# Optimization experiments

Hardware: AMD Instinct MI355X
Metric: run time of the kernel (lower is better)

The kernel has to match this reference:

```python
import jax, jax.numpy as jnp
import numpy as np

H = 16  # n_heads
D = 64  # d_keys


def setup_inputs() -> dict:
    key = jax.random.key(0)
    ks = jax.random.split(key, 11)
    b, n, dm = 2, 2048, 1024
    s = 1.0 / np.sqrt(dm)
    return {
        "q": jax.random.normal(ks[0], (b, n, dm), jnp.float32),
        "k": jax.random.normal(ks[1], (b, n, dm), jnp.float32),
        "v": jax.random.normal(ks[2], (b, n, dm), jnp.float32),
        "Wq": jax.random.normal(ks[3], (dm, H * D), jnp.float32) * s,
        "bq": jax.random.normal(ks[4], (H * D,), jnp.float32) * 0.01,
        "Wk": jax.random.normal(ks[5], (dm, H * D), jnp.float32) * s,
        "bk": jax.random.normal(ks[6], (H * D,), jnp.float32) * 0.01,
        "Wv": jax.random.normal(ks[7], (dm, H * D), jnp.float32) * s,
        "bv": jax.random.normal(ks[8], (H * D,), jnp.float32) * 0.01,
        "Wo": jax.random.normal(ks[9], (H * D, dm), jnp.float32) * s,
        "bo": jax.random.normal(ks[10], (dm,), jnp.float32) * 0.01,
    }


def reference(q, k, v, Wq, bq, Wk, bk, Wv, bv, Wo, bo):
    b, n_q, _ = q.shape
    n_k = k.shape[1]
    # projections -> [b, n, h, d]
    qh = (q @ Wq + bq).reshape(b, n_q, H, D)
    kh = (k @ Wk + bk).reshape(b, n_k, H, D)
    vh = (v @ Wv + bv).reshape(b, n_k, H, D)
    # scores [b, h, n, m]
    scores = jnp.einsum('bnhd,bmhd->bhnm', qh, kh)
    causal = jnp.triu(jnp.ones((n_q, n_k), dtype=bool), k=1)  # True above diag
    scores = jnp.where(causal, -jnp.inf, scores)
    att = jax.nn.softmax(scores / np.sqrt(D).astype(np.float32), axis=-1)
    att_out = jnp.einsum('bhnm,bmhd->bnhd', att, vh).reshape(b, n_q, H * D)
    return att_out @ Wo + bo
```

## Files before the change

### kernel.cpp

```cpp
#include <hip/hip_runtime.h>

typedef float f32x4 __attribute__((ext_vector_type(4)));
typedef __bf16 bf16x8 __attribute__((ext_vector_type(8)));
typedef __bf16 bf16x4 __attribute__((ext_vector_type(4)));
typedef __bf16 bf16_t;

#define NH 16
#define DH 64
#define SEQ 2048
#define DM 1024

#define QSCALE 0.18033688f

extern "C" hipError_t hipMemPtrGetInfo(void* ptr, size_t* size);

__device__ __forceinline__ bf16x8 ld8(const bf16_t* p) { return *(const bf16x8*)p; }
__device__ __forceinline__ void st8(bf16_t* p, bf16x8 v) { *(bf16x8*)p = v; }

__device__ __forceinline__ void gl_lds16(const bf16_t* g, bf16_t* l)
{
    __builtin_amdgcn_global_load_lds(
        (const __attribute__((address_space(1))) unsigned int*)g,
        (__attribute__((address_space(3))) unsigned int*)l, 16, 0, 0);
}

__global__ __launch_bounds__(256) void fill_sentinel(float* out, unsigned n, float val)
{
    unsigned stride = gridDim.x * blockDim.x;
    for (unsigned i = blockIdx.x * blockDim.x + threadIdx.x; i < n; i += stride)
        out[i] = val;
}

__global__ __launch_bounds__(256) void prep(
    const float* __restrict__ q, const float* __restrict__ k,
    const float* __restrict__ v,
    const float* __restrict__ w0, const float* __restrict__ w1,
    const float* __restrict__ w2, const float* __restrict__ w3,
    bf16_t* __restrict__ xb, bf16_t* __restrict__ wt, int fragmode)
{
    int z = blockIdx.z;
    if (z < 3) {
        const float* src = (z == 0) ? q : (z == 1) ? k : v;
        bf16_t* dst = xb + (size_t)z * (4096u * 1024u);
        size_t i8 = ((size_t)blockIdx.x * 256 + threadIdx.x) * 8;
        f32x4 u = *(const f32x4*)(src + i8);
        f32x4 w = *(const f32x4*)(src + i8 + 4);
        bf16x8 h = { (bf16_t)u.x, (bf16_t)u.y, (bf16_t)u.z, (bf16_t)u.w,
                     (bf16_t)w.x, (bf16_t)w.y, (bf16_t)w.z, (bf16_t)w.w };
        st8(dst + i8, h);
    } else {
        int x = blockIdx.x;
        if (x >= 1024) return;
        int w = x >> 8, rem = x & 255;
        int bx = rem & 15, by = rem >> 4;
        const float* in = (w == 0) ? w0 : (w == 1) ? w1 : (w == 2) ? w2 : w3;
        bf16_t* out = wt + (size_t)w * DM * DM;
        __shared__ __align__(16) bf16_t tile[64][72];
        int t = threadIdx.x;
        int k0 = by * 64, n0 = bx * 64;
        int r0 = t >> 4, c0 = (t & 15) * 4;
        for (int p = 0; p < 4; p++) {
            int r = r0 + p * 16;
            const float* src = in + (size_t)(k0 + r) * DM + n0 + c0;
            for (int i = 0; i < 4; i++) tile[r][c0 + i] = (bf16_t)src[i];
        }
        __syncthreads();
        if (fragmode) {
            int idx = t;
            #pragma unroll
            for (int p = 0; p < 2; p++, idx += 256) {
                int rn = idx & 63;
                int kc8 = idx >> 6;
                int n_abs = n0 + rn;
                int rblk = n_abs >> 4, l16v = n_abs & 15;
                int kk = kc8 >> 2, gg = kc8 & 3;
                bf16x8 vv;
                for (int j = 0; j < 8; j++) vv[j] = tile[kc8 * 8 + j][rn];
                st8(out + (size_t)((rblk * 16 + by) * 2 + kk) * 512
                        + (gg * 16 + l16v) * 8, vv);
            }
        } else {
            for (int p = 0; p < 4; p++) {
                int rn = r0 + p * 16;
                bf16_t* dst = out + (size_t)(n0 + rn) * DM + k0 + c0;
                for (int i = 0; i < 4; i++) dst[i] = tile[c0 + i][rn];
            }
        }
    }
}

#define LGKM0 asm volatile("s_waitcnt lgkmcnt(0)" ::: "memory")
#define VMC(n) asm volatile("s_waitcnt vmcnt(" #n ")" ::: "memory")
#define BARRIER __builtin_amdgcn_s_barrier()

#define STA(d, h, dk) do { \
    _Pragma("unroll") for (int j = 0; j < 2; j++) \
        gl_lds16(Xp + ((h) * 128 + j * 64) * DM + (dk) * 64, \
                 Ab + sdst0 + ((d) * 2 + (h)) * 8192 + j * 4096); } while (0)
#define RDA(d, h, F) do { \
    _Pragma("unroll") for (int mf = 0; mf < 4; mf++) { \
        F[mf][0] = ld8(Ab + rA0 + ((d) * 2 + (h)) * 8192 + mf * 1024); \
        F[mf][1] = ld8(Ab + rA1 + ((d) * 2 + (h)) * 8192 + mf * 1024); } } while (0)
#define LDB(SET, nh, kto) do { \
    _Pragma("unroll") for (int nf = 0; nf < 2; nf++) \
        _Pragma("unroll") for (int kk = 0; kk < 2; kk++) \
            SET[nf][kk] = ld8(Bp + (nh) * 131072 + nf * 16384 \
                              + (kto) * 1024 + kk * 512); } while (0)
#define MMQ(AF, BF, Q) do { \
    __builtin_amdgcn_s_setprio(1); \
    _Pragma("unroll") for (int mf = 0; mf < 4; mf++) \
        _Pragma("unroll") for (int nf = 0; nf < 2; nf++) { \
            Q[mf][nf] = __builtin_amdgcn_mfma_f32_16x16x32_bf16( \
                AF[mf][0], BF[nf][0], Q[mf][nf], 0, 0, 0); \
            Q[mf][nf] = __builtin_amdgcn_mfma_f32_16x16x32_bf16( \
                AF[mf][1], BF[nf][1], Q[mf][nf], 0, 0, 0); } \
    __builtin_amdgcn_s_setprio(0); } while (0)

__global__ __launch_bounds__(512, 2) void gemm8(
    const bf16_t* __restrict__ xall, const bf16_t* __restrict__ bfall,
    const float* __restrict__ b0v, const float* __restrict__ b1v,
    const float* __restrict__ b2v, bf16_t* __restrict__ outall,
    float* __restrict__ outf, int mode_base, int out_is_f32)
{
    int z = blockIdx.z;
    int mode = mode_base + z;
    int qkv = (mode_base == 0);
    const bf16_t* X  = xall  + (qkv ? (size_t)z * (4096u * 1024u) : 0);
    const bf16_t* Bf = bfall + (qkv ? (size_t)z * (1024u * 1024u) : 0);
    const float* bias = (z == 0) ? b0v : (z == 1) ? b1v : b2v;
    bf16_t* out = outall + (qkv ? (size_t)z * (4096u * 1024u) : 0);

    int m0 = blockIdx.x * 256;
    int n0 = blockIdx.y * 256;

    __shared__ __align__(16) bf16_t Ab[2 * 2 * 128 * 64];

    int tid  = threadIdx.x;
    int lane = tid & 63, w = tid >> 6;
    int g = lane >> 4, l16 = lane & 15;
    int wm = w >> 2, wn = w & 3;
    int rl = lane >> 3, cl = lane & 7;
    int w8 = w * 8;

    int srow = w8 + rl;
    int scol = (cl ^ rl) * 8;
    const bf16_t* Xp = X + (size_t)(m0 + srow) * DM + scol;
    int sdst0 = w8 * 64 + lane * 8;

    int x7 = l16 & 7;
    int rA0 = (wm * 64 + l16) * 64 + ((0 + g) ^ x7) * 8;
    int rA1 = (wm * 64 + l16) * 64 + ((4 + g) ^ x7) * 8;

    const bf16_t* Bp = Bf + ((size_t)(n0 >> 4) + wn * 2) * 16384 + lane * 8;

    f32x4 a00[4][2] = {}, a01[4][2] = {}, a10[4][2] = {}, a11[4][2] = {};
    bf16x8 afA[4][2], afB[4][2], Ba[2][2], Bb[2][2];

    STA(0, 0, 0); STA(0, 1, 0); STA(1, 0, 1); STA(1, 1, 1);
    LDB(Ba, 0, 0); LDB(Bb, 1, 0);
    VMC(0);
    BARRIER;
    RDA(0, 0, afA);

    #pragma unroll 1
    for (int i = 0; i < 7; i++) {
        VMC(6); LGKM0; MMQ(afA, Ba, a00); BARRIER;
        STA(0, 0, 2); VMC(4); RDA(0, 1, afB); MMQ(afA, Bb, a01); BARRIER;
        LGKM0; MMQ(afB, Ba, a10); LDB(Ba, 0, 1); BARRIER;
        MMQ(afB, Bb, a11); LDB(Bb, 1, 1); STA(0, 1, 2); RDA(1, 0, afA); BARRIER;
        VMC(6); LGKM0; MMQ(afA, Ba, a00); BARRIER;
        STA(1, 0, 3); VMC(4); RDA(1, 1, afB); MMQ(afA, Bb, a01); BARRIER;
        LGKM0; MMQ(afB, Ba, a10); LDB(Ba, 0, 2); BARRIER;
        MMQ(afB, Bb, a11); LDB(Bb, 1, 2); STA(1, 1, 3); RDA(0, 0, afA); BARRIER;
        Xp += 128; Bp += 2048;
    }
    VMC(6); LGKM0; MMQ(afA, Ba, a00); BARRIER;
    VMC(2); RDA(0, 1, afB); MMQ(afA, Bb, a01); BARRIER;
    LGKM0; MMQ(afB, Ba, a10); LDB(Ba, 0, 1); BARRIER;
    MMQ(afB, Bb, a11); LDB(Bb, 1, 1); RDA(1, 0, afA); BARRIER;
    VMC(4); LGKM0; MMQ(afA, Ba, a00); BARRIER;
    VMC(0); RDA(1, 1, afB); MMQ(afA, Bb, a01); BARRIER;
    LGKM0; MMQ(afB, Ba, a10); BARRIER;
    MMQ(afB, Bb, a11);

    float scale = (mode == 0) ? QSCALE : 1.0f;
#define EPI(Q, Mh, Nh) do { \
    _Pragma("unroll") for (int mf = 0; mf < 4; mf++) { \
        int mbase = m0 + (Mh) * 128 + wm * 64 + mf * 16 + g * 4; \
        int bb = mbase >> 11, nn0 = mbase & 2047; \
        _Pragma("unroll") for (int nf = 0; nf < 2; nf++) { \
            int col = n0 + (Nh) * 128 + wn * 32 + nf * 16 + l16; \
            float bv = bias[col]; \
            int hh = col >> 6, dd = col & 63; \
            if (mode == 2) { \
                bf16x4 pv; \
                for (int r = 0; r < 4; r++) pv[r] = (bf16_t)(Q[mf][nf][r] + bv); \
                *(bf16x4*)(out + ((size_t)(bb * NH + hh) * DH + dd) * SEQ + nn0) = pv; \
            } else if (mode == 3) { \
                for (int r = 0; r < 4; r++) { \
                    float sv = Q[mf][nf][r] + bv; \
                    if (out_is_f32) outf[(size_t)(mbase + r) * 1024 + col] = sv; \
                    else            out[(size_t)(mbase + r) * 1024 + col] = (bf16_t)sv; \
                } \
            } else { \
                for (int r = 0; r < 4; r++) \
                    out[((size_t)(bb * NH + hh) * SEQ + nn0 + r) * DH + dd] = \
                        (bf16_t)((Q[mf][nf][r] + bv) * scale); \
            } } } } while (0)
    EPI(a00, 0, 0); EPI(a01, 0, 1); EPI(a10, 1, 0); EPI(a11, 1, 1);
#undef EPI
}

__global__ __launch_bounds__(256) void gemm_mha(
    const float* __restrict__ x0, const float* __restrict__ x1,
    const float* __restrict__ x2, const bf16_t* __restrict__ xb,
    const bf16_t* __restrict__ wt_base,
    const float* __restrict__ b0, const float* __restrict__ b1,
    const float* __restrict__ b2, bf16_t* __restrict__ out_base,
    float* __restrict__ outf, int mode_base, int out_is_f32)
{
    int z = blockIdx.z;
    const float* Xf    = (z == 0) ? x0 : (z == 1) ? x1 : x2;
    const bf16_t* WT   = wt_base + (size_t)z * DM * DM;
    const float* bias  = (z == 0) ? b0 : (z == 1) ? b1 : b2;
    bf16_t* out = out_base + (size_t)z * (4096u * 1024u);
    int mode = mode_base + z;

    int m0 = blockIdx.x * 128;
    int n0 = blockIdx.y * 128;

    __shared__ __align__(16) bf16_t Alds[128 * 64];
    __shared__ __align__(16) bf16_t Blds[128 * 64];

    int t = threadIdx.x;
    int lane = t & 63, wave = t >> 6;
    int g = lane >> 4, l16 = lane & 15;
    int wr0 = (wave >> 1) * 64, wc0 = (wave & 1) * 64;

    f32x4 acc[4][4] = {};
    int srow = t >> 3, sk = (t & 7) * 8;

    for (int k0 = 0; k0 < DM; k0 += 64) {
        __syncthreads();
        if (mode < 3) {
            for (int p = 0; p < 4; p++) {
                int r = srow + p * 32;
                const float* s4 = Xf + (size_t)(m0 + r) * DM + k0 + sk;
                f32x4 u = *(const f32x4*)s4;
                f32x4 w = *(const f32x4*)(s4 + 4);
                bf16x8 h = { (bf16_t)u.x, (bf16_t)u.y, (bf16_t)u.z, (bf16_t)u.w,
                             (bf16_t)w.x, (bf16_t)w.y, (bf16_t)w.z, (bf16_t)w.w };
                st8(Alds + r * 64 + sk, h);
            }
        } else {
            for (int p = 0; p < 4; p++) {
                int r = srow + p * 32;
                st8(Alds + r * 64 + sk, ld8(xb + (size_t)(m0 + r) * DM + k0 + sk));
            }
        }
        for (int p = 0; p < 4; p++) {
            int r = srow + p * 32;
            st8(Blds + r * 64 + sk, ld8(WT + (size_t)(n0 + r) * DM + k0 + sk));
        }
        __syncthreads();
        for (int kk = 0; kk < 2; kk++) {
            bf16x8 af[4], bfr[4];
            for (int i = 0; i < 4; i++)
                af[i] = ld8(Alds + (wr0 + i * 16 + l16) * 64 + kk * 32 + g * 8);
            for (int i = 0; i < 4; i++)
                bfr[i] = ld8(Blds + (wc0 + i * 16 + l16) * 64 + kk * 32 + g * 8);
            for (int mi = 0; mi < 4; mi++)
                for (int ni = 0; ni < 4; ni++)
                    acc[mi][ni] = __builtin_amdgcn_mfma_f32_16x16x32_bf16(
                        af[mi], bfr[ni], acc[mi][ni], 0, 0, 0);
        }
    }
    float scale = (mode == 0) ? QSCALE : 1.0f;
    for (int mi = 0; mi < 4; mi++) {
        int mbase = m0 + wr0 + mi * 16 + g * 4;
        for (int ni = 0; ni < 4; ni++) {
            int col = n0 + wc0 + ni * 16 + l16;
            float bv = bias[col];
            if (mode == 2) {
                int bb = mbase >> 11, nn0 = mbase & 2047;
                int h = col >> 6, d = col & 63;
                bf16x4 pv;
                for (int r = 0; r < 4; r++) pv[r] = (bf16_t)(acc[mi][ni][r] + bv);
                *(bf16x4*)(out + ((size_t)(bb * NH + h) * DH + d) * SEQ + nn0) = pv;
            } else {
                for (int r = 0; r < 4; r++) {
                    int mr = mbase + r;
                    float sv = (acc[mi][ni][r] + bv) * scale;
                    if (mode == 3) {
                        if (out_is_f32) outf[(size_t)mr * 1024 + col] = sv;
                        else            out[(size_t)mr * 1024 + col] = (bf16_t)sv;
                    } else {
                        int bb = mr >> 11, nn = mr & 2047;
                        int h = col >> 6, d = col & 63;
                        out[((size_t)(bb * NH + h) * SEQ + nn) * DH + d] = (bf16_t)sv;
                    }
                }
            }
        }
    }
}

__global__ __launch_bounds__(512) void attn(
    const bf16_t* __restrict__ Qh, const bf16_t* __restrict__ Kh,
    const bf16_t* __restrict__ VT, bf16_t* __restrict__ att)
{
    int bhx = blockIdx.x;
    int yy  = blockIdx.y;
    int p   = (yy < 8) ? yy : 23 - yy;
    int TB  = 2 * p + 2;

    const bf16_t* Qb = Qh + (size_t)bhx * SEQ * DH;
    const bf16_t* Kb = Kh + (size_t)bhx * SEQ * DH;
    const bf16_t* Vb = VT + (size_t)bhx * DH * SEQ;

    __shared__ __align__(16) bf16_t Klds[2][64 * 72];
    __shared__ __align__(16) bf16_t Vlds[2][64 * 72];
    __shared__ __align__(16) bf16_t Plds[8][16 * 72];

    int t = threadIdx.x, lane = t & 63, wave = t >> 6;
    int g = lane >> 4, l16 = lane & 15;
    int srow = t >> 3, sk = (t & 7) * 8;
    int qt = 2 * p + (wave >> 2);
    int Tw = qt + 1;
    int rowl = (wave & 3) * 16 + l16;

    bf16x8 qf[2];
    for (int kk = 0; kk < 2; kk++)
        qf[kk] = ld8(Qb + (size_t)(qt * 64 + rowl) * DH + kk * 32 + g * 8);

    f32x4 accO[4] = {};
    float l = 0.f;
    bf16_t* Pw = Plds[wave];

    st8(&Klds[0][srow * 72 + sk], ld8(Kb + (size_t)srow * DH + sk));
    st8(&Vlds[0][srow * 72 + sk], ld8(Vb + (size_t)srow * SEQ + sk));

    for (int j = 0; j < TB; j++) {
        __syncthreads();
        bool pre = (j + 1 < TB);
        bf16x8 kreg, vreg;
        if (pre) {
            kreg = ld8(Kb + (size_t)((j + 1) * 64 + srow) * DH + sk);
            vreg = ld8(Vb + (size_t)srow * SEQ + (j + 1) * 64 + sk);
        }
        if (j < Tw) {
            int buf = j & 1;
            bool diag = (j == Tw - 1);

            f32x4 s[4];
            __builtin_amdgcn_s_setprio(1);
            for (int c = 0; c < 4; c++) {
                f32x4 a = {};
                for (int kk = 0; kk < 2; kk++) {
                    bf16x8 kf = ld8(&Klds[buf][(c * 16 + l16) * 72 + kk * 32 + g * 8]);
                    a = __builtin_amdgcn_mfma_f32_16x16x32_bf16(kf, qf[kk], a, 0, 0, 0);
                }
                s[c] = a;
            }
            __builtin_amdgcn_s_setprio(0);
            for (int c = 0; c < 4; c++) {
                bf16x4 pv;
                for (int r = 0; r < 4; r++) {
                    float v = s[c][r];
                    if (diag && (c * 16 + g * 4 + r) > rowl) v = -1e30f;
                    float pe = exp2f(v);
                    l += pe;
                    pv[r] = (bf16_t)pe;
                }
                *(bf16x4*)(Pw + l16 * 72 + c * 16 + g * 4) = pv;
            }
            asm volatile("s_waitcnt lgkmcnt(0)" ::: "memory");

            bf16x8 pf0 = ld8(Pw + l16 * 72 + g * 8);
            bf16x8 pf1 = ld8(Pw + l16 * 72 + 32 + g * 8);
            __builtin_amdgcn_s_setprio(1);
            for (int c2 = 0; c2 < 4; c2++) {
                bf16x8 vf0 = ld8(&Vlds[buf][(c2 * 16 + l16) * 72 + g * 8]);
                accO[c2] = __builtin_amdgcn_mfma_f32_16x16x32_bf16(vf0, pf0, accO[c2], 0, 0, 0);
                bf16x8 vf1 = ld8(&Vlds[buf][(c2 * 16 + l16) * 72 + 32 + g * 8]);
                accO[c2] = __builtin_amdgcn_mfma_f32_16x16x32_bf16(vf1, pf1, accO[c2], 0, 0, 0);
            }
            __builtin_amdgcn_s_setprio(0);

            if (diag) {
                float lt = l;
                lt += __shfl_xor(lt, 16);
                lt += __shfl_xor(lt, 32);
                float inv = 1.f / lt;
                int qabs = qt * 64 + rowl;
                int bb = bhx >> 4, h = bhx & 15;
                for (int c2 = 0; c2 < 4; c2++) {
                    bf16x4 ov;
                    for (int r = 0; r < 4; r++) ov[r] = (bf16_t)(accO[c2][r] * inv);
                    *(bf16x4*)(att + (((size_t)bb * SEQ + qabs) * NH + h) * DH
                               + c2 * 16 + g * 4) = ov;
                }
            }
        }
        if (pre) {
            int b = (j + 1) & 1;
            st8(&Klds[b][srow * 72 + sk], kreg);
            st8(&Vlds[b][srow * 72 + sk], vreg);
        }
    }
}

extern "C" void kernel_launch(void* const* d_in, const int* in_sizes, int n_in,
                              void* d_out, int out_size, void* d_ws, size_t ws_size,
                              hipStream_t stream) {
    const float* q  = (const float*)d_in[0];
    const float* k  = (const float*)d_in[1];
    const float* v  = (const float*)d_in[2];
    const float* Wq = (const float*)d_in[3];
    const float* bq = (const float*)d_in[4];
    const float* Wk = (const float*)d_in[5];
    const float* bk = (const float*)d_in[6];
    const float* Wv = (const float*)d_in[7];
    const float* bv = (const float*)d_in[8];
    const float* Wo = (const float*)d_in[9];
    const float* bo = (const float*)d_in[10];

    const size_t MAT = 1024u * 1024u;
    const size_t BIG = 4096u * 1024u;
    const size_t NEED_BASE = 64 + (4 * BIG + 4 * MAT) * 2;
    const size_t NEED_FAST = NEED_BASE + 3 * BIG * 2;

    if (ws_size < NEED_BASE) {
        fill_sentinel<<<1024, 256, 0, stream>>>((float*)d_out,
                                                (unsigned)out_size, 100.0f);
        return;
    }

    int out_is_f32 = 1;
    size_t osz = 0;
    if (hipMemPtrGetInfo(d_out, &osz) == hipSuccess && osz != 0 &&
        osz < (size_t)out_size * 4)
        out_is_f32 = 0;

    bf16_t* base = (bf16_t*)d_ws + 32;
    bf16_t* Qh  = base;
    bf16_t* Kh  = Qh + BIG;
    bf16_t* VT  = Kh + BIG;
    bf16_t* att = VT + BIG;
    bf16_t* WT  = att + BIG;
    bf16_t* Xb  = WT + 4 * MAT;

    if (ws_size >= NEED_FAST) {
        prep<<<dim3(2048, 1, 4), 256, 0, stream>>>(q, k, v, Wq, Wk, Wv, Wo,
                                                   Xb, WT, 1);
        gemm8<<<dim3(16, 4, 3), 512, 0, stream>>>(Xb, WT, bq, bk, bv,
                                                  Qh, nullptr, 0, 0);
        attn<<<dim3(32, 16), 512, 0, stream>>>(Qh, Kh, VT, att);
        gemm8<<<dim3(16, 4, 1), 512, 0, stream>>>(att, WT + 3 * MAT,
                                                  bo, bo, bo,
                                                  (bf16_t*)d_out, (float*)d_out,
                                                  3, out_is_f32);
    } else {
        prep<<<dim3(2048, 1, 4), 256, 0, stream>>>(q, k, v, Wq, Wk, Wv, Wo,
                                                   (bf16_t*)d_ws, WT, 0);
        gemm_mha<<<dim3(32, 8, 3), 256, 0, stream>>>(q, k, v, nullptr, WT,
                                                     bq, bk, bv, Qh, nullptr, 0, 0);
        attn<<<dim3(32, 16), 512, 0, stream>>>(Qh, Kh, VT, att);
        gemm_mha<<<dim3(32, 8, 1), 256, 0, stream>>>(nullptr, nullptr, nullptr, att,
                                                     WT + 3 * MAT, bo, bo, bo,
                                                     (bf16_t*)d_out, (float*)d_out,
                                                     3, out_is_f32);
    }
}
```

Measured before the change: 239.6 us.

## Use dedicated 128x128-tile kernel for output projection and raw v_exp in attention

The output projection no longer reuses the 256x256-tile gemm8 kernel, which launched only 64 blocks. It now runs in a new gemm_out kernel with 128x128 tiles over 256 blocks, to fill more of the GPU's compute units. Because gemm_out expects a plain row-major transposed Wo layout, the prep kernel stops writing Wo in fragment layout. The attention softmax also replaces exp2f with inline v_exp_f32 assembly to avoid libm range handling. The new kernel is simple and single-buffered with no load/compute overlap, so per-block efficiency may be lower than the pipelined gemm8.

```diff
diff --git a/kernel.cpp b/kernel.cpp
--- a/kernel.cpp
+++ b/kernel.cpp
@@ -65,7 +65,7 @@
             for (int i = 0; i < 4; i++) tile[r][c0 + i] = (bf16_t)src[i];
         }
         __syncthreads();
-        if (fragmode) {
+        if (fragmode && w < 3) {
             int idx = t;
             #pragma unroll
             for (int p = 0; p < 2; p++, idx += 256) {
@@ -119,16 +119,14 @@
 __global__ __launch_bounds__(512, 2) void gemm8(
     const bf16_t* __restrict__ xall, const bf16_t* __restrict__ bfall,
     const float* __restrict__ b0v, const float* __restrict__ b1v,
-    const float* __restrict__ b2v, bf16_t* __restrict__ outall,
-    float* __restrict__ outf, int mode_base, int out_is_f32)
+    const float* __restrict__ b2v, bf16_t* __restrict__ outall)
 {
     int z = blockIdx.z;
-    int mode = mode_base + z;
-    int qkv = (mode_base == 0);
-    const bf16_t* X  = xall  + (qkv ? (size_t)z * (4096u * 1024u) : 0);
-    const bf16_t* Bf = bfall + (qkv ? (size_t)z * (1024u * 1024u) : 0);
+    int mode = z;
+    const bf16_t* X  = xall  + (size_t)z * (4096u * 1024u);
+    const bf16_t* Bf = bfall + (size_t)z * (1024u * 1024u);
     const float* bias = (z == 0) ? b0v : (z == 1) ? b1v : b2v;
-    bf16_t* out = outall + (qkv ? (size_t)z * (4096u * 1024u) : 0);
+    bf16_t* out = outall + (size_t)z * (4096u * 1024u);
 
     int m0 = blockIdx.x * 256;
     int n0 = blockIdx.y * 256;
@@ -196,12 +194,6 @@
                 bf16x4 pv; \
                 for (int r = 0; r < 4; r++) pv[r] = (bf16_t)(Q[mf][nf][r] + bv); \
                 *(bf16x4*)(out + ((size_t)(bb * NH + hh) * DH + dd) * SEQ + nn0) = pv; \
-            } else if (mode == 3) { \
-                for (int r = 0; r < 4; r++) { \
-                    float sv = Q[mf][nf][r] + bv; \
-                    if (out_is_f32) outf[(size_t)(mbase + r) * 1024 + col] = sv; \
-                    else            out[(size_t)(mbase + r) * 1024 + col] = (bf16_t)sv; \
-                } \
             } else { \
                 for (int r = 0; r < 4; r++) \
                     out[((size_t)(bb * NH + hh) * SEQ + nn0 + r) * DH + dd] = \
@@ -209,6 +201,62 @@
             } } } } while (0)
     EPI(a00, 0, 0); EPI(a01, 0, 1); EPI(a10, 1, 0); EPI(a11, 1, 1);
 #undef EPI
+}
+
+__global__ __launch_bounds__(256) void gemm_out(
+    const bf16_t* __restrict__ X, const bf16_t* __restrict__ WT,
+    const float* __restrict__ bias, bf16_t* __restrict__ out,
+    float* __restrict__ outf, int out_is_f32)
+{
+    int m0 = blockIdx.x * 128;
+    int n0 = blockIdx.y * 128;
+
+    __shared__ __align__(16) bf16_t Alds[128 * 64];
+    __shared__ __align__(16) bf16_t Blds[128 * 64];
+
+    int t = threadIdx.x;
+    int lane = t & 63, wave = t >> 6;
+    int g = lane >> 4, l16 = lane & 15;
+    int wr0 = (wave >> 1) * 64, wc0 = (wave & 1) * 64;
+    int crow = lane >> 3;
+    int ccol = (lane & 7) * 8;
+
+    f32x4 acc[4][4] = {};
+
+    for (int k0 = 0; k0 < DM; k0 += 64) {
+        __syncthreads();
+        for (int c = wave; c < 16; c += 4) {
+            int row = c * 8 + crow;
+            gl_lds16(X  + (size_t)(m0 + row) * DM + k0 + ccol,
+                     Alds + c * 512 + lane * 8);
+            gl_lds16(WT + (size_t)(n0 + row) * DM + k0 + ccol,
+                     Blds + c * 512 + lane * 8);
+        }
+        __syncthreads();
+        for (int kk = 0; kk < 2; kk++) {
+            bf16x8 af[4], bfr[4];
+            for (int i = 0; i < 4; i++)
+                af[i] = ld8(Alds + (wr0 + i * 16 + l16) * 64 + kk * 32 + g * 8);
+            for (int i = 0; i < 4; i++)
+                bfr[i] = ld8(Blds + (wc0 + i * 16 + l16) * 64 + kk * 32 + g * 8);
+            for (int mi = 0; mi < 4; mi++)
+                for (int ni = 0; ni < 4; ni++)
+                    acc[mi][ni] = __builtin_amdgcn_mfma_f32_16x16x32_bf16(
+                        af[mi], bfr[ni], acc[mi][ni], 0, 0, 0);
+        }
+    }
+    for (int mi = 0; mi < 4; mi++) {
+        int mbase = m0 + wr0 + mi * 16 + g * 4;
+        for (int ni = 0; ni < 4; ni++) {
+            int col = n0 + wc0 + ni * 16 + l16;
+            float bv = bias[col];
+            for (int r = 0; r < 4; r++) {
+                float sv = acc[mi][ni][r] + bv;
+                if (out_is_f32) outf[(size_t)(mbase + r) * 1024 + col] = sv;
+                else            out[(size_t)(mbase + r) * 1024 + col] = (bf16_t)sv;
+            }
+        }
+    }
 }
 
 __global__ __launch_bounds__(256) void gemm_mha(
@@ -368,7 +416,8 @@
                 for (int r = 0; r < 4; r++) {
                     float v = s[c][r];
                     if (diag && (c * 16 + g * 4 + r) > rowl) v = -1e30f;
-                    float pe = exp2f(v);
+                    float pe;
+                    asm("v_exp_f32 %0, %1" : "=v"(pe) : "v"(v));
                     l += pe;
                     pv[r] = (bf16_t)pe;
                 }
@@ -453,13 +502,11 @@
     if (ws_size >= NEED_FAST) {
         prep<<<dim3(2048, 1, 4), 256, 0, stream>>>(q, k, v, Wq, Wk, Wv, Wo,
                                                    Xb, WT, 1);
-        gemm8<<<dim3(16, 4, 3), 512, 0, stream>>>(Xb, WT, bq, bk, bv,
-                                                  Qh, nullptr, 0, 0);
+        gemm8<<<dim3(16, 4, 3), 512, 0, stream>>>(Xb, WT, bq, bk, bv, Qh);
         attn<<<dim3(32, 16), 512, 0, stream>>>(Qh, Kh, VT, att);
-        gemm8<<<dim3(16, 4, 1), 512, 0, stream>>>(att, WT + 3 * MAT,
-                                                  bo, bo, bo,
+        gemm_out<<<dim3(32, 8), 256, 0, stream>>>(att, WT + 3 * MAT, bo,
                                                   (bf16_t*)d_out, (float*)d_out,
-                                                  3, out_is_f32);
+                                                  out_is_f32);
     } else {
         prep<<<dim3(2048, 1, 4), 256, 0, stream>>>(q, k, v, Wq, Wk, Wv, Wo,
                                                    (bf16_t*)d_ws, WT, 0);
```

Measured after the change: 225.2 us. 1.06x faster.
